# Kernel tuning notes

Measured on AMD Instinct MI355X. Metric: run time of the kernel, lower is better.

## Reference

```python
import jax, jax.numpy as jnp
import numpy as np

N_NODES, E_TOT, E_ACT = 20000, 250000, 200000
LAT, OH = 128, 128
M0, M1, M2 = 64, 32, 16            # irreps_out: 64x0e + 32x1o + 16x2e
D_IR = M0 + 3 * M1 + 5 * M2        # 240
G = M1 + M2                        # gate scalars (48)
T0 = M0 + G                        # tp m=0 scalar channels (112)
I0, I1, I2 = 3 * M0, 3 * M1, 3 * M2  # tp input muls (center|edge|neighbor)


def _split(x, m0, m1, m2):
    e = x.shape[0]
    return (x[:, :m0],
            x[:, m0:m0 + 3 * m1].reshape(e, m1, 3),
            x[:, m0 + 3 * m1:].reshape(e, m2, 5))


def _merge(s0, s1, s2):
    e = s0.shape[0]
    return jnp.concatenate([s0, s1.reshape(e, -1), s2.reshape(e, -1)], axis=-1)


def _mlp(x, ws, bs):
    for i, (w, b) in enumerate(zip(ws, bs)):
        x = x @ w + b
        if i < len(ws) - 1:
            x = jax.nn.silu(x)
    return x


def _forward(latents, node_features, edge_features, cutoff_coeffs, edge_one_hot,
             wigner_D1, wigner_D2,
             W0, W1r, W1i, W2r, W2i, Gw, Gb,
             P0, P0b, P1, P2, Ew, Eb, ln_g, ln_b,
             A1, A1b, A2, A2b, A3, A3b,
             B1, B1b, B2, B2b, B3, B3b,
             O0, O1, O2,
             edge_index, active_edges):
    ec = edge_index[0][active_edges]
    en = edge_index[1][active_edges]
    # gather node features per edge (equivariant_norm_type='none' -> identity norms)
    nc0, nc1, nc2 = _split(node_features[ec], M0, M1, M2)
    ef0, ef1, ef2 = _split(edge_features, M0, M1, M2)
    nn0, nn1, nn2 = _split(node_features[en], M0, M1, M2)
    x0 = jnp.concatenate([nc0, ef0, nn0], -1)   # [E,192]
    x1 = jnp.concatenate([nc1, ef1, nn1], 1)    # [E,96,3]
    x2 = jnp.concatenate([nc2, ef2, nn2], 1)    # [E,48,5]
    lat_a = latents[active_edges]
    # --- SO(2) linear: rotate into edge frame, per-m mixing, latent gains, rotate back ---
    r1 = jnp.einsum('eij,euj->eui', wigner_D1, x1)
    r2 = jnp.einsum('eij,euj->eui', wigner_D2, x2)
    in0 = jnp.concatenate([x0, r1[:, :, 1], r2[:, :, 2]], -1)   # m=0 [E,336]
    o_m0 = in0 @ W0.T                                           # [E,160]
    ip1 = jnp.concatenate([r1[:, :, 2], r2[:, :, 3]], -1)       # m=+1 [E,144]
    im1 = jnp.concatenate([r1[:, :, 0], r2[:, :, 1]], -1)       # m=-1
    op1 = ip1 @ W1r.T - im1 @ W1i.T                             # [E,48]
    on1 = ip1 @ W1i.T + im1 @ W1r.T
    op2 = r2[:, :, 4] @ W2r.T - r2[:, :, 0] @ W2i.T             # [E,16]
    on2 = r2[:, :, 4] @ W2i.T + r2[:, :, 0] @ W2r.T
    g = lat_a @ Gw + Gb                                         # per-edge gains [E,224]
    o_m0 = o_m0 * g[:, :160]
    g1 = g[:, 160:208]; g2 = g[:, 208:224]
    op1 = op1 * g1; on1 = on1 * g1; op2 = op2 * g2; on2 = on2 * g2
    y0 = o_m0[:, :T0]
    y1 = jnp.stack([on1[:, :M1], o_m0[:, T0:T0 + M1], op1[:, :M1]], -1)          # [E,32,3]
    y2 = jnp.stack([on2, on1[:, M1:], o_m0[:, T0 + M1:], op1[:, M1:], op2], -1)  # [E,16,5]
    y1 = jnp.einsum('eji,euj->eui', wigner_D1, y1)
    y2 = jnp.einsum('eji,euj->eui', wigner_D2, y2)
    # --- gate activation ---
    gates = jax.nn.sigmoid(y0[:, M0:])
    z0 = jax.nn.silu(y0[:, :M0])
    z1 = y1 * gates[:, :M1, None]
    z2 = y2 * gates[:, M1:, None]
    # --- lin_post: per-l channel mixing, fan-in normalized, bias on scalars ---
    z0 = z0 @ P0.T / np.sqrt(M0) + P0b
    z1 = jnp.einsum('uv,evm->eum', P1, z1) / np.sqrt(M1)
    z2 = jnp.einsum('uv,evm->eum', P2, z2) / np.sqrt(M2)
    scalars = z0                                               # taken before weighting
    # --- E3ElementLinear: per-edge per-channel weights from latents ---
    w = lat_a @ Ew + Eb                                        # [E,112]
    z0 = z0 * w[:, :M0]
    z1 = z1 * w[:, M0:M0 + M1, None]
    z2 = z2 * w[:, M0 + M1:, None]
    new_edge = _merge(z0, z1, z2)
    # --- latent update: LN -> mlp1(ln_lat||scalars) -> mlp2(h||one_hot) -> cutoff ---
    mu = lat_a.mean(-1, keepdims=True)
    var = ((lat_a - mu) ** 2).mean(-1, keepdims=True)
    ln_lat = (lat_a - mu) * jax.lax.rsqrt(var + 1e-5) * ln_g + ln_b
    h = _mlp(jnp.concatenate([ln_lat, scalars], -1), (A1, A2, A3), (A1b, A2b, A3b))
    h = _mlp(jnp.concatenate([h, edge_one_hot], -1), (B1, B2, B3), (B1b, B2b, B3b))
    new_lat = cutoff_coeffs[active_edges][:, None] * h
    # --- residual update (res_update_params buffer = 0) ---
    u = jax.nn.sigmoid(jnp.asarray(0.0, new_edge.dtype))
    c_old = jax.lax.rsqrt(u * u + 1.0)
    c_new = u * c_old
    edge_out = c_old * edge_features + c_new * new_edge        # identity residual path
    latents_out = latents.at[active_edges].set(c_new * new_lat + c_old * lat_a)
    # --- layer one-hot tensor product (uvu with 128x0e) ---
    f0, f1, f2 = _split(edge_out, M0, M1, M2)
    s = 1.0 / np.sqrt(OH)
    t0 = f0 * (edge_one_hot @ O0.T) * s
    t1 = f1 * (edge_one_hot @ O1.T)[:, :, None] * s
    t2 = f2 * (edge_one_hot @ O2.T)[:, :, None] * s
    edge_out = edge_out + _merge(t0, t1, t2)
    return edge_out, latents_out


def setup_inputs() -> dict:
    key = jax.random.key(0)
    ks = iter(jax.random.split(key, 64))
    nrm = lambda sh, s=0.05: jax.random.normal(next(ks), sh, jnp.float32) * s
    inp = dict(
        latents=nrm((E_TOT, LAT), 1.0),
        node_features=nrm((N_NODES, D_IR), 1.0),
        edge_features=nrm((E_ACT, D_IR), 1.0),
        cutoff_coeffs=jax.random.uniform(next(ks), (E_TOT,), jnp.float32),
        edge_one_hot=jax.random.uniform(next(ks), (E_ACT, OH), jnp.float32),
        wigner_D1=nrm((E_ACT, 3, 3), 0.5),
        wigner_D2=nrm((E_ACT, 5, 5), 0.3),
        W0=nrm((160, I0 + I1 + I2)), W1r=nrm((48, 144)), W1i=nrm((48, 144)),
        W2r=nrm((16, 48)), W2i=nrm((16, 48)),
        Gw=nrm((LAT, 224)), Gb=jnp.ones((224,), jnp.float32),
        P0=nrm((M0, M0)), P0b=nrm((M0,)), P1=nrm((M1, M1)), P2=nrm((M2, M2)),
        Ew=nrm((LAT, M0 + M1 + M2)), Eb=jnp.ones((M0 + M1 + M2,), jnp.float32),
        ln_g=jnp.ones((LAT,), jnp.float32), ln_b=jnp.zeros((LAT,), jnp.float32),
        A1=nrm((LAT + M0, LAT)), A1b=nrm((LAT,)),
        A2=nrm((LAT, LAT)), A2b=nrm((LAT,)),
        A3=nrm((LAT, LAT)), A3b=nrm((LAT,)),
        B1=nrm((LAT + OH, LAT)), B1b=nrm((LAT,)),
        B2=nrm((LAT, LAT)), B2b=nrm((LAT,)),
        B3=nrm((LAT, LAT)), B3b=nrm((LAT,)),
        O0=nrm((M0, OH)), O1=nrm((M1, OH)), O2=nrm((M2, OH)),
        edge_index=jax.random.randint(next(ks), (2, E_TOT), 0, N_NODES, jnp.int32),
        active_edges=jnp.sort(jax.random.permutation(next(ks), E_TOT)[:E_ACT]).astype(jnp.int32),
    )
    return inp


def reference(latents, node_features, edge_features, cutoff_coeffs, edge_one_hot,
              wigner_D1, wigner_D2,
              W0, W1r, W1i, W2r, W2i, Gw, Gb,
              P0, P0b, P1, P2, Ew, Eb, ln_g, ln_b,
              A1, A1b, A2, A2b, A3, A3b,
              B1, B1b, B2, B2b, B3, B3b,
              O0, O1, O2, edge_index, active_edges):
    return _forward(latents, node_features, edge_features, cutoff_coeffs, edge_one_hot,
                    wigner_D1, wigner_D2,
                    W0, W1r, W1i, W2r, W2i, Gw, Gb,
                    P0, P0b, P1, P2, Ew, Eb, ln_g, ln_b,
                    A1, A1b, A2, A2b, A3, A3b,
                    B1, B1b, B2, B2b, B3, B3b,
                    O0, O1, O2, edge_index, active_edges)
```

## Files before the change

### kernel.cpp

```cpp
#include <hip/hip_runtime.h>

typedef unsigned short us_t;
typedef short bf16x8 __attribute__((ext_vector_type(8)));
typedef float f32x4 __attribute__((ext_vector_type(4)));

#define E_ACT 200000
#define E_TOT 250000
#define DIR   240
#define C_OLD 0.8944271909999159f
#define C_NEW 0.4472135954999579f
#define S_OH  0.08838834764831845f

#define WO_W0   0
#define WO_W1P  56320
#define WO_W1M  70144
#define WO_W2P  83968
#define WO_W2M  85504
#define WO_GW   87040
#define WO_EW   115712
#define WO_A1   130048
#define WO_A2   154624
#define WO_A3   171008
#define WO_B1   187392
#define WO_B2   220160
#define WO_B3   236544
#define WO_O0   252928
#define WO_O1   261120
#define WO_O2   265216
#define WO_P0T  267264
#define WO_P1T  271360
#define WO_P2T  272384
#define W_TOTAL 272896

__device__ __forceinline__ float b2f(us_t u) { return __uint_as_float(((unsigned)u) << 16); }
__device__ __forceinline__ us_t f2b(float f) {
    unsigned x = __float_as_uint(f);
    return (us_t)((x + 0x7fffu + ((x >> 16) & 1u)) >> 16);
}
__device__ __forceinline__ float sigm(float x) { return 1.0f / (1.0f + __expf(-x)); }

#define MFMA(a,b,c) __builtin_amdgcn_mfma_f32_16x16x32_bf16((a),(b),(c),0,0,0)

__global__ __launch_bounds__(256) void prep_kernel(
    const float* __restrict__ W0, const float* __restrict__ W1r, const float* __restrict__ W1i,
    const float* __restrict__ W2r, const float* __restrict__ W2i,
    const float* __restrict__ Gw, const float* __restrict__ Ew,
    const float* __restrict__ A1, const float* __restrict__ A2, const float* __restrict__ A3,
    const float* __restrict__ B1, const float* __restrict__ B2, const float* __restrict__ B3,
    const float* __restrict__ O0, const float* __restrict__ O1, const float* __restrict__ O2,
    const float* __restrict__ P0w, const float* __restrict__ P1w, const float* __restrict__ P2w,
    us_t* __restrict__ wb)
{
    int idx = blockIdx.x * 256 + threadIdx.x;
    if (idx >= W_TOTAL) return;
    float v;
    if (idx < WO_W1P) {
        int r = idx, n = r / 352, k = r % 352;
        v = (k < 336) ? W0[n * 336 + k] : 0.f;
    } else if (idx < WO_W1M) {
        int r = idx - WO_W1P, n = r / 288, k = r % 288;
        v = (k < 144) ? W1r[n * 144 + k] : -W1i[n * 144 + (k - 144)];
    } else if (idx < WO_W2P) {
        int r = idx - WO_W1M, n = r / 288, k = r % 288;
        v = (k < 144) ? W1i[n * 144 + k] : W1r[n * 144 + (k - 144)];
    } else if (idx < WO_W2M) {
        int r = idx - WO_W2P, n = r / 96, k = r % 96;
        v = (k < 48) ? W2r[n * 48 + k] : -W2i[n * 48 + (k - 48)];
    } else if (idx < WO_GW) {
        int r = idx - WO_W2M, n = r / 96, k = r % 96;
        v = (k < 48) ? W2i[n * 48 + k] : W2r[n * 48 + (k - 48)];
    } else if (idx < WO_EW) {
        int r = idx - WO_GW, n = r / 128, k = r % 128;
        v = Gw[k * 224 + n];
    } else if (idx < WO_A1) {
        int r = idx - WO_EW, n = r / 128, k = r % 128;
        v = Ew[k * 112 + n];
    } else if (idx < WO_A2) {
        int r = idx - WO_A1, n = r / 192, k = r % 192;
        v = A1[k * 128 + n];
    } else if (idx < WO_A3) {
        int r = idx - WO_A2, n = r / 128, k = r % 128;
        v = A2[k * 128 + n];
    } else if (idx < WO_B1) {
        int r = idx - WO_A3, n = r / 128, k = r % 128;
        v = A3[k * 128 + n];
    } else if (idx < WO_B2) {
        int r = idx - WO_B1, n = r / 256, k = r % 256;
        v = B1[k * 128 + n];
    } else if (idx < WO_B3) {
        int r = idx - WO_B2, n = r / 128, k = r % 128;
        v = B2[k * 128 + n];
    } else if (idx < WO_O0) {
        int r = idx - WO_B3, n = r / 128, k = r % 128;
        v = B3[k * 128 + n];
    } else if (idx < WO_O1) {
        v = O0[idx - WO_O0];
    } else if (idx < WO_O2) {
        v = O1[idx - WO_O1];
    } else if (idx < WO_P0T) {
        v = O2[idx - WO_O2];
    } else if (idx < WO_P1T) {
        v = P0w[idx - WO_P0T];
    } else if (idx < WO_P2T) {
        v = P1w[idx - WO_P1T];
    } else {
        int r = idx - WO_P2T, n = r / 32, k = r % 32;
        v = (k < 16) ? P2w[n * 16 + k] : 0.f;
    }
    wb[idx] = f2b(v);
}

__global__ __launch_bounds__(256) void kcopy_kernel(
    const float* __restrict__ latents, const int* __restrict__ act,
    float* __restrict__ out_lat)
{
    int idx = blockIdx.x * 256 + threadIdx.x;
    if (idx >= E_TOT * 16) return;
    int row = idx >> 4, part = idx & 15;
    int lo = 0, hi = E_ACT;
    while (lo < hi) {
        int mid = (lo + hi) >> 1;
        if (act[mid] < row) lo = mid + 1; else hi = mid;
    }
    bool active = (lo < E_ACT) && (act[lo] == row);
    if (!active) {
        const float4* src = (const float4*)&latents[(size_t)row * 128 + part * 8];
        float4* dst = (float4*)&out_lat[(size_t)row * 128 + part * 8];
        dst[0] = src[0];
        dst[1] = src[1];
    }
}

__device__ __forceinline__ void lat_fetch_a(const float* __restrict__ latents,
                                            const int* __restrict__ aes_l,
                                            int lane, bf16x8 a[4])
{
    const int r = lane & 15, g = lane >> 4;
    const float* lp = latents + (size_t)aes_l[r] * 128 + g * 8;
    #pragma unroll
    for (int ks = 0; ks < 4; ++ks) {
        float4 v0 = *(const float4*)(lp + ks * 32);
        float4 v1 = *(const float4*)(lp + ks * 32 + 4);
        bf16x8 av;
        av[0] = (short)f2b(v0.x); av[1] = (short)f2b(v0.y);
        av[2] = (short)f2b(v0.z); av[3] = (short)f2b(v0.w);
        av[4] = (short)f2b(v1.x); av[5] = (short)f2b(v1.y);
        av[6] = (short)f2b(v1.z); av[7] = (short)f2b(v1.w);
        a[ks] = av;
    }
}

__device__ __forceinline__ void gemmW0g32(
    const us_t* __restrict__ in0s, const us_t* __restrict__ wbase,
    const bf16x8 lA[4], const bf16x8 lB[4], const float* __restrict__ Gb,
    int nt, us_t* __restrict__ om0g, int lane)
{
    const int r = lane & 15, g = lane >> 4;
    f32x4 wa = {0.f,0.f,0.f,0.f}, wb = wa, ga = wa, gb = wa;
    const us_t* apA = in0s + r * 360 + g * 8;
    const us_t* apB = in0s + (16 + r) * 360 + g * 8;
    const us_t* wp  = wbase + WO_W0 + (size_t)(nt * 16 + r) * 352 + g * 8;
    #pragma unroll
    for (int ks = 0; ks < 11; ++ks) {
        bf16x8 b = *(const bf16x8*)(wp + ks * 32);
        wa = MFMA(*(const bf16x8*)(apA + ks * 32), b, wa);
        wb = MFMA(*(const bf16x8*)(apB + ks * 32), b, wb);
    }
    const us_t* gp = wbase + WO_GW + (size_t)(nt * 16 + r) * 128 + g * 8;
    #pragma unroll
    for (int ks = 0; ks < 4; ++ks) {
        bf16x8 b = *(const bf16x8*)(gp + ks * 32);
        ga = MFMA(lA[ks], b, ga);
        gb = MFMA(lB[ks], b, gb);
    }
    float bi = Gb[nt * 16 + r];
    #pragma unroll
    for (int i = 0; i < 4; ++i) {
        int eA = g * 4 + i, eB = 16 + g * 4 + i;
        om0g[eA * 162 + nt * 16 + r] = f2b(wa[i] * (ga[i] + bi));
        om0g[eB * 162 + nt * 16 + r] = f2b(wb[i] * (gb[i] + bi));
    }
}

__device__ __forceinline__ void gemmW1g32(
    const us_t* __restrict__ cact1, const us_t* __restrict__ wbase,
    const bf16x8 lA[4], const bf16x8 lB[4], const float* __restrict__ Gb,
    int j, us_t* __restrict__ cp1g, us_t* __restrict__ cn1g, int lane)
{
    const int r = lane & 15, g = lane >> 4;
    f32x4 pa = {0.f,0.f,0.f,0.f}, pb = pa, ma = pa, mb = pa, ga = pa, gb = pa;
    const us_t* apA = cact1 + r * 296 + g * 8;
    const us_t* apB = cact1 + (16 + r) * 296 + g * 8;
    const us_t* wpP = wbase + WO_W1P + (size_t)(j * 16 + r) * 288 + g * 8;
    const us_t* wpM = wbase + WO_W1M + (size_t)(j * 16 + r) * 288 + g * 8;
    #pragma unroll
    for (int ks = 0; ks < 9; ++ks) {
        bf16x8 aA = *(const bf16x8*)(apA + ks * 32);
        bf16x8 aB = *(const bf16x8*)(apB + ks * 32);
        bf16x8 bP = *(const bf16x8*)(wpP + ks * 32);
        bf16x8 bM = *(const bf16x8*)(wpM + ks * 32);
        pa = MFMA(aA, bP, pa); pb = MFMA(aB, bP, pb);
        ma = MFMA(aA, bM, ma); mb = MFMA(aB, bM, mb);
    }
    const us_t* gp = wbase + WO_GW + (size_t)(160 + j * 16 + r) * 128 + g * 8;
    #pragma unroll
    for (int ks = 0; ks < 4; ++ks) {
        bf16x8 b = *(const bf16x8*)(gp + ks * 32);
        ga = MFMA(lA[ks], b, ga);
        gb = MFMA(lB[ks], b, gb);
    }
    float bi = Gb[160 + j * 16 + r];
    #pragma unroll
    for (int i = 0; i < 4; ++i) {
        int eA = g * 4 + i, eB = 16 + g * 4 + i;
        float gA = ga[i] + bi, gB = gb[i] + bi;
        cp1g[eA * 50 + j * 16 + r] = f2b(pa[i] * gA);
        cn1g[eA * 50 + j * 16 + r] = f2b(ma[i] * gA);
        cp1g[eB * 50 + j * 16 + r] = f2b(pb[i] * gB);
        cn1g[eB * 50 + j * 16 + r] = f2b(mb[i] * gB);
    }
}

__device__ __forceinline__ void gemmW2g32(
    const us_t* __restrict__ cact2, const us_t* __restrict__ wbase,
    const bf16x8 lA[4], const bf16x8 lB[4], const float* __restrict__ Gb,
    us_t* __restrict__ cp2g, us_t* __restrict__ cn2g, int lane)
{
    const int r = lane & 15, g = lane >> 4;
    f32x4 pa = {0.f,0.f,0.f,0.f}, pb = pa, ma = pa, mb = pa, ga = pa, gb = pa;
    const us_t* apA = cact2 + r * 104 + g * 8;
    const us_t* apB = cact2 + (16 + r) * 104 + g * 8;
    const us_t* wpP = wbase + WO_W2P + (size_t)r * 96 + g * 8;
    const us_t* wpM = wbase + WO_W2M + (size_t)r * 96 + g * 8;
    #pragma unroll
    for (int ks = 0; ks < 3; ++ks) {
        bf16x8 aA = *(const bf16x8*)(apA + ks * 32);
        bf16x8 aB = *(const bf16x8*)(apB + ks * 32);
        bf16x8 bP = *(const bf16x8*)(wpP + ks * 32);
        bf16x8 bM = *(const bf16x8*)(wpM + ks * 32);
        pa = MFMA(aA, bP, pa); pb = MFMA(aB, bP, pb);
        ma = MFMA(aA, bM, ma); mb = MFMA(aB, bM, mb);
    }
    const us_t* gp = wbase + WO_GW + (size_t)(208 + r) * 128 + g * 8;
    #pragma unroll
    for (int ks = 0; ks < 4; ++ks) {
        bf16x8 b = *(const bf16x8*)(gp + ks * 32);
        ga = MFMA(lA[ks], b, ga);
        gb = MFMA(lB[ks], b, gb);
    }
    float bi = Gb[208 + r];
    #pragma unroll
    for (int i = 0; i < 4; ++i) {
        int eA = g * 4 + i, eB = 16 + g * 4 + i;
        float gA = ga[i] + bi, gB = gb[i] + bi;
        cp2g[eA * 18 + r] = f2b(pa[i] * gA);
        cn2g[eA * 18 + r] = f2b(ma[i] * gA);
        cp2g[eB * 18 + r] = f2b(pb[i] * gB);
        cn2g[eB * 18 + r] = f2b(mb[i] * gB);
    }
}

__device__ __forceinline__ void lat_gemmE32(
    const bf16x8 lA[4], const bf16x8 lB[4],
    const us_t* __restrict__ wgt, const float* __restrict__ bias,
    int nt, us_t* __restrict__ wl, int lane)
{
    const int r = lane & 15, g = lane >> 4;
    f32x4 aA = {0.f,0.f,0.f,0.f}, aB = aA;
    const us_t* wp = wgt + (size_t)(nt * 16 + r) * 128 + g * 8;
    #pragma unroll
    for (int ks = 0; ks < 4; ++ks) {
        bf16x8 b = *(const bf16x8*)(wp + ks * 32);
        aA = MFMA(lA[ks], b, aA);
        aB = MFMA(lB[ks], b, aB);
    }
    float bi = bias[nt * 16 + r];
    #pragma unroll
    for (int i = 0; i < 4; ++i) {
        int eA = g * 4 + i, eB = 16 + g * 4 + i;
        wl[eA * 120 + nt * 16 + r] = f2b(aA[i] + bi);
        wl[eB * 120 + nt * 16 + r] = f2b(aB[i] + bi);
    }
}

template<int KS>
__device__ __forceinline__ void pgemm32(const us_t* __restrict__ actbase, int as,
                                        const us_t* __restrict__ wgt, int kp, int lane,
                                        f32x4& accA, f32x4& accB)
{
    const int r = lane & 15, g = lane >> 4;
    const us_t* apA = actbase + r * as + g * 8;
    const us_t* apB = actbase + (16 + r) * as + g * 8;
    const us_t* wp = wgt + (size_t)r * kp + g * 8;
    #pragma unroll
    for (int ks = 0; ks < KS; ++ks) {
        bf16x8 b = *(const bf16x8*)(wp + ks * 32);
        accA = MFMA(*(const bf16x8*)(apA + ks * 32), b, accA);
        accB = MFMA(*(const bf16x8*)(apB + ks * 32), b, accB);
    }
}

template<int KS, bool SILU>
__device__ __forceinline__ void mlayer(
    const us_t* __restrict__ actA, const us_t* __restrict__ actB, int split, int as,
    const us_t* __restrict__ wgt, int kp, const float* __restrict__ bias,
    us_t* __restrict__ out, int os, int lane, int w)
{
    const int r = lane & 15, g = lane >> 4;
    const int n0 = 2 * w * 16, n1 = n0 + 16;
    f32x4 a00 = {0.f,0.f,0.f,0.f}, a01 = a00, a10 = a00, a11 = a00;
    const us_t* wp0 = wgt + (size_t)(n0 + r) * kp + g * 8;
    const us_t* wp1 = wgt + (size_t)(n1 + r) * kp + g * 8;
    #pragma unroll
    for (int ks = 0; ks < KS; ++ks) {
        const us_t* ab = (ks < split) ? (actA + ks * 32) : (actB + (ks - split) * 32);
        bf16x8 f0 = *(const bf16x8*)(ab + r * as + g * 8);
        bf16x8 f1 = *(const bf16x8*)(ab + (16 + r) * as + g * 8);
        bf16x8 b0 = *(const bf16x8*)(wp0 + ks * 32);
        bf16x8 b1 = *(const bf16x8*)(wp1 + ks * 32);
        a00 = MFMA(f0, b0, a00); a01 = MFMA(f0, b1, a01);
        a10 = MFMA(f1, b0, a10); a11 = MFMA(f1, b1, a11);
    }
    float bi0 = bias[n0 + r], bi1 = bias[n1 + r];
    #pragma unroll
    for (int i = 0; i < 4; ++i) {
        int eA = g * 4 + i, eB = 16 + g * 4 + i;
        float v;
        v = a00[i] + bi0; if (SILU) v *= sigm(v); out[eA * os + n0 + r] = f2b(v);
        v = a01[i] + bi1; if (SILU) v *= sigm(v); out[eA * os + n1 + r] = f2b(v);
        v = a10[i] + bi0; if (SILU) v *= sigm(v); out[eB * os + n0 + r] = f2b(v);
        v = a11[i] + bi1; if (SILU) v *= sigm(v); out[eB * os + n1 + r] = f2b(v);
    }
}

__global__ __launch_bounds__(256, 2) void fused_kernel(
    const float* __restrict__ latents,
    const float* __restrict__ node_features,
    const float* __restrict__ edge_features,
    const float* __restrict__ cutoff,
    const float* __restrict__ one_hot,
    const float* __restrict__ wD1,
    const float* __restrict__ wD2,
    const float* __restrict__ Gb,  const float* __restrict__ Eb,
    const float* __restrict__ P0b,
    const float* __restrict__ ln_g, const float* __restrict__ ln_b,
    const float* __restrict__ A1b, const float* __restrict__ A2b, const float* __restrict__ A3b,
    const float* __restrict__ B1b, const float* __restrict__ B2b, const float* __restrict__ B3b,
    const int* __restrict__ edge_index, const int* __restrict__ active_edges,
    const us_t* __restrict__ wbase,
    us_t* __restrict__ ne_ws,
    float* __restrict__ out_edge, float* __restrict__ out_lat)
{
    __shared__ __align__(16) char smem[80640];
    us_t* in0s  = (us_t*)(smem);
    us_t* cact1 = (us_t*)(smem + 23040);
    us_t* cact2 = (us_t*)(smem + 41984);
    us_t* z0l   = (us_t*)(smem);
    us_t* z1l   = (us_t*)(smem + 4608);
    us_t* z2l   = (us_t*)(smem + 11264);
    us_t* x_lds = (us_t*)(smem);
    us_t* h_a   = (us_t*)(smem + 12800);
    us_t* h_b   = (us_t*)(smem + 21504);
    us_t* ohl   = (us_t*)(smem + 30208);
    us_t* ohw_l = (us_t*)(smem + 38912);
    float* D1l  = (float*)(smem + 48640);
    float* D2l  = (float*)(smem + 50176);
    int*   aes  = (int*)(smem + 53760);
    us_t* om0g  = (us_t*)(smem + 53888);
    us_t* cp1g  = (us_t*)(smem + 64256);
    us_t* cn1g  = (us_t*)(smem + 67456);
    us_t* cp2g  = (us_t*)(smem + 70656);
    us_t* cn2g  = (us_t*)(smem + 71808);
    us_t* wl    = (us_t*)(smem + 72960);
    us_t* scal_l= (us_t*)(smem + 64256);
    float* cut_l= (float*)(smem + 53888);

    const int t  = threadIdx.x;
    const int e0 = blockIdx.x * 32;
    const int lane = t & 63, w = t >> 6;

    #pragma unroll
    for (int ep = 0; ep < 2; ++ep) {
        const int e = (t >> 4) + 16 * ep, l = t & 15;
        const int eg = e0 + e;
        const int ae = active_edges[eg];
        const int ec = edge_index[ae];
        const int en = edge_index[E_TOT + ae];
        if (l == 0) aes[e] = ae;

        float v1  = (l < 9) ? wD1[(size_t)eg * 9 + l] : 0.f;
        float v2a = wD2[(size_t)eg * 25 + l];
        float v2b = (l < 9) ? wD2[(size_t)eg * 25 + 16 + l] : 0.f;
        if (l < 9) D1l[e * 12 + l] = v1;
        D2l[e * 28 + l] = v2a;
        if (l < 9) D2l[e * 28 + 16 + l] = v2b;

        float d1[9], d2[25];
        #pragma unroll
        for (int i = 0; i < 9; ++i)  d1[i] = __shfl(v1, i, 16);
        #pragma unroll
        for (int i = 0; i < 16; ++i) d2[i] = __shfl(v2a, i, 16);
        #pragma unroll
        for (int i = 0; i < 9; ++i)  d2[16 + i] = __shfl(v2b, i, 16);

        const float* pc = node_features + (size_t)ec * DIR;
        const float* pe = edge_features + (size_t)eg * DIR;
        const float* pn = node_features + (size_t)en * DIR;
        us_t* in0 = in0s + e * 360;
        us_t* c1  = cact1 + e * 296;
        us_t* c2  = cact2 + e * 104;

        #pragma unroll
        for (int j = 0; j < 4; ++j) {
            int i = l + 16 * j;
            in0[i]       = f2b(pc[i]);
            in0[64 + i]  = f2b(pe[i]);
            in0[128 + i] = f2b(pn[i]);
        }
        in0[336 + l] = 0;

        #pragma unroll
        for (int jj = 0; jj < 6; ++jj) {
            int u = l + 16 * jj;
            int uu = u & 31;
            const float* sp = (u < 32 ? pc : (u < 64 ? pe : pn)) + 64 + uu * 3;
            float x0 = sp[0], x1 = sp[1], x2 = sp[2];
            float r0 = d1[0] * x0 + d1[1] * x1 + d1[2] * x2;
            float r1 = d1[3] * x0 + d1[4] * x1 + d1[5] * x2;
            float r2 = d1[6] * x0 + d1[7] * x1 + d1[8] * x2;
            c1[144 + u]  = f2b(r0);
            in0[192 + u] = f2b(r1);
            c1[u]        = f2b(r2);
        }
        #pragma unroll
        for (int jj = 0; jj < 3; ++jj) {
            int u = l + 16 * jj;
            int uu = u & 15;
            const float* sp = (u < 16 ? pc : (u < 32 ? pe : pn)) + 160 + uu * 5;
            float x0 = sp[0], x1 = sp[1], x2 = sp[2], x3 = sp[3], x4 = sp[4];
            float r[5];
            #pragma unroll
            for (int i = 0; i < 5; ++i)
                r[i] = d2[i * 5 + 0] * x0 + d2[i * 5 + 1] * x1 + d2[i * 5 + 2] * x2
                     + d2[i * 5 + 3] * x3 + d2[i * 5 + 4] * x4;
            c2[48 + u]   = f2b(r[0]);
            c1[240 + u]  = f2b(r[1]);
            in0[288 + u] = f2b(r[2]);
            c1[96 + u]   = f2b(r[3]);
            c2[u]        = f2b(r[4]);
        }
    }
    __syncthreads();

    {
        bf16x8 lA[4], lB[4];
        lat_fetch_a(latents, aes, lane, lA);
        lat_fetch_a(latents, aes + 16, lane, lB);
        if (w == 0) {
            gemmW0g32(in0s, wbase, lA, lB, Gb, 0, om0g, lane);
            gemmW0g32(in0s, wbase, lA, lB, Gb, 1, om0g, lane);
            gemmW0g32(in0s, wbase, lA, lB, Gb, 2, om0g, lane);
            gemmW1g32(cact1, wbase, lA, lB, Gb, 0, cp1g, cn1g, lane);
        } else if (w == 1) {
            gemmW0g32(in0s, wbase, lA, lB, Gb, 3, om0g, lane);
            gemmW0g32(in0s, wbase, lA, lB, Gb, 4, om0g, lane);
            gemmW0g32(in0s, wbase, lA, lB, Gb, 5, om0g, lane);
            gemmW1g32(cact1, wbase, lA, lB, Gb, 1, cp1g, cn1g, lane);
        } else if (w == 2) {
            gemmW0g32(in0s, wbase, lA, lB, Gb, 6, om0g, lane);
            gemmW0g32(in0s, wbase, lA, lB, Gb, 7, om0g, lane);
            gemmW0g32(in0s, wbase, lA, lB, Gb, 8, om0g, lane);
            gemmW1g32(cact1, wbase, lA, lB, Gb, 2, cp1g, cn1g, lane);
        } else {
            gemmW0g32(in0s, wbase, lA, lB, Gb, 9, om0g, lane);
            gemmW2g32(cact2, wbase, lA, lB, Gb, cp2g, cn2g, lane);
            #pragma unroll
            for (int nt = 0; nt < 7; ++nt)
                lat_gemmE32(lA, lB, wbase + WO_EW, Eb, nt, wl, lane);
        }
    }
    __syncthreads();

    #pragma unroll
    for (int ep = 0; ep < 2; ++ep) {
        const int e = (t >> 4) + 16 * ep, l = t & 15;
        const float* D1e = D1l + e * 12;
        const float* D2e = D2l + e * 28;
        #pragma unroll
        for (int uu = 0; uu < 2; ++uu) {
            int u = l + uu * 16;
            float j0 = b2f(cn1g[e * 50 + u]);
            float j1 = b2f(om0g[e * 162 + 112 + u]);
            float j2 = b2f(cp1g[e * 50 + u]);
            float gate = sigm(b2f(om0g[e * 162 + 64 + u]));
            #pragma unroll
            for (int i = 0; i < 3; ++i) {
                float yr = D1e[0 * 3 + i] * j0 + D1e[1 * 3 + i] * j1 + D1e[2 * 3 + i] * j2;
                z1l[e * 104 + i * 32 + u] = f2b(yr * gate);
            }
        }
        {
            int u = l;
            float j0 = b2f(cn2g[e * 18 + u]);
            float j1 = b2f(cn1g[e * 50 + 32 + u]);
            float j2 = b2f(om0g[e * 162 + 144 + u]);
            float j3 = b2f(cp1g[e * 50 + 32 + u]);
            float j4 = b2f(cp2g[e * 18 + u]);
            float gate = sigm(b2f(om0g[e * 162 + 96 + u]));
            #pragma unroll
            for (int i = 0; i < 5; ++i) {
                float yr = D2e[0 * 5 + i] * j0 + D2e[1 * 5 + i] * j1 + D2e[2 * 5 + i] * j2
                         + D2e[3 * 5 + i] * j3 + D2e[4 * 5 + i] * j4;
                z2l[e * 168 + i * 32 + u] = f2b(yr * gate);
                z2l[e * 168 + i * 32 + 16 + u] = 0;
            }
        }
        #pragma unroll
        for (int ii = 0; ii < 4; ++ii) {
            int c = l + 16 * ii;
            float v = b2f(om0g[e * 162 + c]);
            z0l[e * 72 + c] = f2b(v * sigm(v));
        }
    }
    __syncthreads();

    {
        const int r = lane & 15, g = lane >> 4;
        const float sc1 = 0.17677669529663687f;
        if (w < 2) {
            #pragma unroll
            for (int jj = 0; jj < 2; ++jj) {
                int nt = 2 * w + jj;
                f32x4 aA = {0.f,0.f,0.f,0.f}, aB = aA;
                pgemm32<2>(z0l, 72, wbase + WO_P0T + nt * 16 * 64, 64, lane, aA, aB);
                int n = nt * 16 + r;
                float bi = P0b[n];
                #pragma unroll
                for (int i = 0; i < 4; ++i) {
                    int eA = g * 4 + i, eB = 16 + g * 4 + i;
                    float zA = aA[i] * 0.125f + bi;
                    float zB = aB[i] * 0.125f + bi;
                    scal_l[eA * 64 + n] = f2b(zA);
                    scal_l[eB * 64 + n] = f2b(zB);
                    ne_ws[(size_t)(e0 + eA) * 240 + n] = f2b(zA * b2f(wl[eA * 120 + n]));
                    ne_ws[(size_t)(e0 + eB) * 240 + n] = f2b(zB * b2f(wl[eB * 120 + n]));
                }
            }
        } else if (w == 2) {
            #pragma unroll
            for (int m = 0; m < 3; ++m) {
                #pragma unroll
                for (int nt = 0; nt < 2; ++nt) {
                    f32x4 aA = {0.f,0.f,0.f,0.f}, aB = aA;
                    pgemm32<1>(z1l + m * 32, 104, wbase + WO_P1T + nt * 16 * 32, 32,
                               lane, aA, aB);
                    int u = nt * 16 + r;
                    #pragma unroll
                    for (int i = 0; i < 4; ++i) {
                        int eA = g * 4 + i, eB = 16 + g * 4 + i;
                        ne_ws[(size_t)(e0 + eA) * 240 + 64 + u * 3 + m] =
                            f2b(aA[i] * sc1 * b2f(wl[eA * 120 + 64 + u]));
                        ne_ws[(size_t)(e0 + eB) * 240 + 64 + u * 3 + m] =
                            f2b(aB[i] * sc1 * b2f(wl[eB * 120 + 64 + u]));
                    }
                }
            }
        } else if (w == 3) {
            #pragma unroll
            for (int m = 0; m < 5; ++m) {
                f32x4 aA = {0.f,0.f,0.f,0.f}, aB = aA;
                pgemm32<1>(z2l + m * 32, 168, wbase + WO_P2T, 32, lane, aA, aB);
                int u = r;
                #pragma unroll
                for (int i = 0; i < 4; ++i) {
                    int eA = g * 4 + i, eB = 16 + g * 4 + i;
                    ne_ws[(size_t)(e0 + eA) * 240 + 160 + u * 5 + m] =
                        f2b(aA[i] * 0.25f * b2f(wl[eA * 120 + 96 + u]));
                    ne_ws[(size_t)(e0 + eB) * 240 + 160 + u * 5 + m] =
                        f2b(aB[i] * 0.25f * b2f(wl[eB * 120 + 96 + u]));
                }
            }
        }
    }
    __syncthreads();

    {
        int ee = t >> 3, l8 = t & 7;
        int ae = aes[ee];
        if (l8 == 0) cut_l[ee] = cutoff[ae];
        const float* lp = latents + (size_t)ae * 128 + l8 * 16;
        float xs[16];
        #pragma unroll
        for (int q = 0; q < 4; ++q) {
            float4 v = *(const float4*)(lp + q * 4);
            xs[q * 4 + 0] = v.x; xs[q * 4 + 1] = v.y;
            xs[q * 4 + 2] = v.z; xs[q * 4 + 3] = v.w;
        }
        float s1 = 0.f, s2 = 0.f;
        #pragma unroll
        for (int i = 0; i < 16; ++i) { s1 += xs[i]; s2 += xs[i] * xs[i]; }
        #pragma unroll
        for (int off = 1; off < 8; off <<= 1) {
            s1 += __shfl_xor(s1, off, 8);
            s2 += __shfl_xor(s2, off, 8);
        }
        float mu  = s1 * (1.f / 128.f);
        float var = s2 * (1.f / 128.f) - mu * mu;
        float rstd = rsqrtf(var + 1e-5f);
        #pragma unroll
        for (int i = 0; i < 16; ++i) {
            int li = l8 * 16 + i;
            x_lds[ee * 200 + li] = f2b((xs[i] - mu) * rstd * ln_g[li] + ln_b[li]);
        }
        #pragma unroll
        for (int q = 0; q < 2; ++q) {
            int j = l8 * 2 + q;
            *(ushort4*)&x_lds[ee * 200 + 128 + j * 4] =
                *(const ushort4*)&scal_l[ee * 64 + j * 4];
        }
    }
    for (int idx = t; idx < 32 * 32; idx += 256) {
        int ee = idx >> 5, j = idx & 31;
        float4 ov = *(const float4*)&one_hot[(size_t)(e0 + ee) * 128 + j * 4];
        ushort4 s; s.x = f2b(ov.x); s.y = f2b(ov.y); s.z = f2b(ov.z); s.w = f2b(ov.w);
        *(ushort4*)&ohl[ee * 136 + j * 4] = s;
    }
    __syncthreads();

    mlayer<6, true>(x_lds, x_lds, 6, 200, wbase + WO_A1, 192, A1b, h_a, 136, lane, w);
    __syncthreads();
    mlayer<4, true>(h_a, h_a, 4, 136, wbase + WO_A2, 128, A2b, h_b, 136, lane, w);
    __syncthreads();
    mlayer<4, false>(h_b, h_b, 4, 136, wbase + WO_A3, 128, A3b, h_a, 136, lane, w);
    __syncthreads();
    mlayer<8, true>(h_a, ohl, 4, 136, wbase + WO_B1, 256, B1b, h_b, 136, lane, w);
    __syncthreads();
    mlayer<4, true>(h_b, h_b, 4, 136, wbase + WO_B2, 128, B2b, h_a, 136, lane, w);
    __syncthreads();

    {
        const int r = lane & 15, g = lane >> 4;
        const int n0 = 2 * w * 16, n1 = n0 + 16;
        f32x4 a00 = {0.f,0.f,0.f,0.f}, a01 = a00, a10 = a00, a11 = a00;
        const us_t* wp0 = wbase + WO_B3 + (size_t)(n0 + r) * 128 + g * 8;
        const us_t* wp1 = wbase + WO_B3 + (size_t)(n1 + r) * 128 + g * 8;
        #pragma unroll
        for (int ks = 0; ks < 4; ++ks) {
            bf16x8 f0 = *(const bf16x8*)(h_a + ks * 32 + r * 136 + g * 8);
            bf16x8 f1 = *(const bf16x8*)(h_a + ks * 32 + (16 + r) * 136 + g * 8);
            bf16x8 b0 = *(const bf16x8*)(wp0 + ks * 32);
            bf16x8 b1 = *(const bf16x8*)(wp1 + ks * 32);
            a00 = MFMA(f0, b0, a00); a01 = MFMA(f0, b1, a01);
            a10 = MFMA(f1, b0, a10); a11 = MFMA(f1, b1, a11);
        }
        float bi0 = B3b[n0 + r], bi1 = B3b[n1 + r];
        #pragma unroll
        for (int i = 0; i < 4; ++i) {
            int eA = g * 4 + i, eB = 16 + g * 4 + i;
            int aeA = aes[eA], aeB = aes[eB];
            float cA = C_NEW * cut_l[eA], cB = C_NEW * cut_l[eB];
            float* oA = out_lat + (size_t)aeA * 128;
            float* oB = out_lat + (size_t)aeB * 128;
            const float* lA = latents + (size_t)aeA * 128;
            const float* lB = latents + (size_t)aeB * 128;
            oA[n0 + r] = cA * (a00[i] + bi0) + C_OLD * lA[n0 + r];
            oA[n1 + r] = cA * (a01[i] + bi1) + C_OLD * lA[n1 + r];
            oB[n0 + r] = cB * (a10[i] + bi0) + C_OLD * lB[n0 + r];
            oB[n1 + r] = cB * (a11[i] + bi1) + C_OLD * lB[n1 + r];
        }
    }
    {
        const int r = lane & 15, g = lane >> 4;
        const int cnt = (w == 3) ? 1 : 2;
        #pragma unroll
        for (int ii = 0; ii < 2; ++ii) {
            if (ii >= cnt) break;
            int nt = (ii == 0) ? w : w + 4;
            const us_t* wb2 = (nt < 4) ? (wbase + WO_O0 + (size_t)nt * 16 * 128)
                            : (nt < 6) ? (wbase + WO_O1 + (size_t)(nt - 4) * 16 * 128)
                                       : (wbase + WO_O2);
            f32x4 c0 = {0.f,0.f,0.f,0.f}, c1 = c0;
            const us_t* wp = wb2 + (size_t)r * 128 + g * 8;
            #pragma unroll
            for (int ks = 0; ks < 4; ++ks) {
                bf16x8 f0 = *(const bf16x8*)(ohl + ks * 32 + r * 136 + g * 8);
                bf16x8 f1 = *(const bf16x8*)(ohl + ks * 32 + (16 + r) * 136 + g * 8);
                bf16x8 b = *(const bf16x8*)(wp + ks * 32);
                c0 = MFMA(f0, b, c0); c1 = MFMA(f1, b, c1);
            }
            int n = nt * 16 + r;
            #pragma unroll
            for (int i = 0; i < 4; ++i) {
                int eA = g * 4 + i, eB = 16 + g * 4 + i;
                ohw_l[eA * 112 + n] = f2b(c0[i]);
                ohw_l[eB * 112 + n] = f2b(c1[i]);
            }
        }
    }
    __syncthreads();

    for (int idx = t; idx < 32 * 60; idx += 256) {
        int e = idx / 60;
        int c0 = (idx - e * 60) * 4;
        size_t eg = (size_t)(e0 + e);
        float4 ef = *(const float4*)&edge_features[eg * 240 + c0];
        ushort4 nv = *(const ushort4*)&ne_ws[eg * 240 + c0];
        float nef[4] = {b2f(nv.x), b2f(nv.y), b2f(nv.z), b2f(nv.w)};
        float eff[4] = {ef.x, ef.y, ef.z, ef.w};
        float4 ov;
        float* op = &ov.x;
        #pragma unroll
        for (int j = 0; j < 4; ++j) {
            int c = c0 + j;
            int o;
            if (c < 64)       o = c;
            else if (c < 160) o = 64 + (c - 64) / 3;
            else              o = 96 + (c - 160) / 5;
            float ohv = b2f(ohw_l[e * 112 + o]);
            op[j] = (C_OLD * eff[j] + C_NEW * nef[j]) * (1.f + S_OH * ohv);
        }
        *(float4*)&out_edge[eg * 240 + c0] = ov;
    }
}

extern "C" void kernel_launch(void* const* d_in, const int* in_sizes, int n_in,
                              void* d_out, int out_size, void* d_ws, size_t ws_size,
                              hipStream_t stream)
{
    const float* latents  = (const float*)d_in[0];
    const float* node_f   = (const float*)d_in[1];
    const float* edge_f   = (const float*)d_in[2];
    const float* cutoff   = (const float*)d_in[3];
    const float* one_hot  = (const float*)d_in[4];
    const float* wD1      = (const float*)d_in[5];
    const float* wD2      = (const float*)d_in[6];
    const float* W0       = (const float*)d_in[7];
    const float* W1r      = (const float*)d_in[8];
    const float* W1i      = (const float*)d_in[9];
    const float* W2r      = (const float*)d_in[10];
    const float* W2i      = (const float*)d_in[11];
    const float* Gw       = (const float*)d_in[12];
    const float* Gb       = (const float*)d_in[13];
    const float* P0w      = (const float*)d_in[14];
    const float* P0b      = (const float*)d_in[15];
    const float* P1w      = (const float*)d_in[16];
    const float* P2w      = (const float*)d_in[17];
    const float* Ew       = (const float*)d_in[18];
    const float* Eb       = (const float*)d_in[19];
    const float* ln_g     = (const float*)d_in[20];
    const float* ln_b     = (const float*)d_in[21];
    const float* A1       = (const float*)d_in[22];
    const float* A1b      = (const float*)d_in[23];
    const float* A2       = (const float*)d_in[24];
    const float* A2b      = (const float*)d_in[25];
    const float* A3       = (const float*)d_in[26];
    const float* A3b      = (const float*)d_in[27];
    const float* B1       = (const float*)d_in[28];
    const float* B1b      = (const float*)d_in[29];
    const float* B2       = (const float*)d_in[30];
    const float* B2b      = (const float*)d_in[31];
    const float* B3       = (const float*)d_in[32];
    const float* B3b      = (const float*)d_in[33];
    const float* O0       = (const float*)d_in[34];
    const float* O1       = (const float*)d_in[35];
    const float* O2       = (const float*)d_in[36];
    const int* edge_index = (const int*)d_in[37];
    const int* act_e      = (const int*)d_in[38];

    float* out_edge = (float*)d_out;
    float* out_lat  = out_edge + (size_t)E_ACT * DIR;

    us_t* ne_ws   = (us_t*)d_ws;
    us_t* wbase   = ne_ws + (size_t)E_ACT * DIR;

    prep_kernel<<<dim3((W_TOTAL + 255) / 256), dim3(256), 0, stream>>>(
        W0, W1r, W1i, W2r, W2i, Gw, Ew, A1, A2, A3, B1, B2, B3,
        O0, O1, O2, P0w, P1w, P2w, wbase);

    kcopy_kernel<<<dim3((E_TOT * 16 + 255) / 256), dim3(256), 0, stream>>>(
        latents, act_e, out_lat);

    fused_kernel<<<dim3(E_ACT / 32), dim3(256), 0, stream>>>(
        latents, node_f, edge_f, cutoff, one_hot, wD1, wD2,
        Gb, Eb, P0b, ln_g, ln_b,
        A1b, A2b, A3b, B1b, B2b, B3b,
        edge_index, act_e, wbase, ne_ws, out_edge, out_lat);
}
```

Measured before the change: 699.3 us.

## Double fused kernel block to 512 threads and redistribute per-wave GEMM work

The fused kernel now runs 8 waves per 32-edge block instead of 4. Each phase (gather/rotate, SO(2) GEMMs, projection GEMMs, layernorm, MLP layers, output heads) is re-partitioned so each wave handles fewer N-tiles or edges, and launch bounds move to (512,4). The goal is more parallelism within each block and lower per-wave register pressure, so latency is better hidden. The cost is that each block still uses about 80 KB of LDS, which limits how many blocks fit per CU, and some phases leave waves poorly balanced.

```diff
diff --git a/kernel.cpp b/kernel.cpp
--- a/kernel.cpp
+++ b/kernel.cpp
@@ -301,39 +301,35 @@
 }
 
 template<int KS, bool SILU>
-__device__ __forceinline__ void mlayer(
+__device__ __forceinline__ void mlayer8(
     const us_t* __restrict__ actA, const us_t* __restrict__ actB, int split, int as,
     const us_t* __restrict__ wgt, int kp, const float* __restrict__ bias,
     us_t* __restrict__ out, int os, int lane, int w)
 {
     const int r = lane & 15, g = lane >> 4;
-    const int n0 = 2 * w * 16, n1 = n0 + 16;
-    f32x4 a00 = {0.f,0.f,0.f,0.f}, a01 = a00, a10 = a00, a11 = a00;
-    const us_t* wp0 = wgt + (size_t)(n0 + r) * kp + g * 8;
-    const us_t* wp1 = wgt + (size_t)(n1 + r) * kp + g * 8;
+    const int n0 = w * 16;
+    f32x4 a0 = {0.f,0.f,0.f,0.f}, a1 = a0;
+    const us_t* wp = wgt + (size_t)(n0 + r) * kp + g * 8;
     #pragma unroll
     for (int ks = 0; ks < KS; ++ks) {
         const us_t* ab = (ks < split) ? (actA + ks * 32) : (actB + (ks - split) * 32);
         bf16x8 f0 = *(const bf16x8*)(ab + r * as + g * 8);
         bf16x8 f1 = *(const bf16x8*)(ab + (16 + r) * as + g * 8);
-        bf16x8 b0 = *(const bf16x8*)(wp0 + ks * 32);
-        bf16x8 b1 = *(const bf16x8*)(wp1 + ks * 32);
-        a00 = MFMA(f0, b0, a00); a01 = MFMA(f0, b1, a01);
-        a10 = MFMA(f1, b0, a10); a11 = MFMA(f1, b1, a11);
-    }
-    float bi0 = bias[n0 + r], bi1 = bias[n1 + r];
+        bf16x8 b = *(const bf16x8*)(wp + ks * 32);
+        a0 = MFMA(f0, b, a0);
+        a1 = MFMA(f1, b, a1);
+    }
+    float bi = bias[n0 + r];
     #pragma unroll
     for (int i = 0; i < 4; ++i) {
         int eA = g * 4 + i, eB = 16 + g * 4 + i;
         float v;
-        v = a00[i] + bi0; if (SILU) v *= sigm(v); out[eA * os + n0 + r] = f2b(v);
-        v = a01[i] + bi1; if (SILU) v *= sigm(v); out[eA * os + n1 + r] = f2b(v);
-        v = a10[i] + bi0; if (SILU) v *= sigm(v); out[eB * os + n0 + r] = f2b(v);
-        v = a11[i] + bi1; if (SILU) v *= sigm(v); out[eB * os + n1 + r] = f2b(v);
-    }
-}
-
-__global__ __launch_bounds__(256, 2) void fused_kernel(
+        v = a0[i] + bi; if (SILU) v *= sigm(v); out[eA * os + n0 + r] = f2b(v);
+        v = a1[i] + bi; if (SILU) v *= sigm(v); out[eB * os + n0 + r] = f2b(v);
+    }
+}
+
+__global__ __launch_bounds__(512, 4) void fused_kernel(
     const float* __restrict__ latents,
     const float* __restrict__ node_features,
     const float* __restrict__ edge_features,
@@ -379,9 +375,8 @@
     const int e0 = blockIdx.x * 32;
     const int lane = t & 63, w = t >> 6;
 
-    #pragma unroll
-    for (int ep = 0; ep < 2; ++ep) {
-        const int e = (t >> 4) + 16 * ep, l = t & 15;
+    {
+        const int e = t >> 4, l = t & 15;
         const int eg = e0 + e;
         const int ae = active_edges[eg];
         const int ec = edge_index[ae];
@@ -456,24 +451,16 @@
         bf16x8 lA[4], lB[4];
         lat_fetch_a(latents, aes, lane, lA);
         lat_fetch_a(latents, aes + 16, lane, lB);
-        if (w == 0) {
-            gemmW0g32(in0s, wbase, lA, lB, Gb, 0, om0g, lane);
-            gemmW0g32(in0s, wbase, lA, lB, Gb, 1, om0g, lane);
-            gemmW0g32(in0s, wbase, lA, lB, Gb, 2, om0g, lane);
+        if (w < 5) {
+            gemmW0g32(in0s, wbase, lA, lB, Gb, 2 * w, om0g, lane);
+            gemmW0g32(in0s, wbase, lA, lB, Gb, 2 * w + 1, om0g, lane);
+        } else if (w == 5) {
             gemmW1g32(cact1, wbase, lA, lB, Gb, 0, cp1g, cn1g, lane);
-        } else if (w == 1) {
-            gemmW0g32(in0s, wbase, lA, lB, Gb, 3, om0g, lane);
-            gemmW0g32(in0s, wbase, lA, lB, Gb, 4, om0g, lane);
-            gemmW0g32(in0s, wbase, lA, lB, Gb, 5, om0g, lane);
             gemmW1g32(cact1, wbase, lA, lB, Gb, 1, cp1g, cn1g, lane);
-        } else if (w == 2) {
-            gemmW0g32(in0s, wbase, lA, lB, Gb, 6, om0g, lane);
-            gemmW0g32(in0s, wbase, lA, lB, Gb, 7, om0g, lane);
-            gemmW0g32(in0s, wbase, lA, lB, Gb, 8, om0g, lane);
+        } else if (w == 6) {
             gemmW1g32(cact1, wbase, lA, lB, Gb, 2, cp1g, cn1g, lane);
+            gemmW2g32(cact2, wbase, lA, lB, Gb, cp2g, cn2g, lane);
         } else {
-            gemmW0g32(in0s, wbase, lA, lB, Gb, 9, om0g, lane);
-            gemmW2g32(cact2, wbase, lA, lB, Gb, cp2g, cn2g, lane);
             #pragma unroll
             for (int nt = 0; nt < 7; ++nt)
                 lat_gemmE32(lA, lB, wbase + WO_EW, Eb, nt, wl, lane);
@@ -481,9 +468,8 @@
     }
     __syncthreads();
 
-    #pragma unroll
-    for (int ep = 0; ep < 2; ++ep) {
-        const int e = (t >> 4) + 16 * ep, l = t & 15;
+    {
+        const int e = t >> 4, l = t & 15;
         const float* D1e = D1l + e * 12;
         const float* D2e = D2l + e * 28;
         #pragma unroll
@@ -527,47 +513,44 @@
     {
         const int r = lane & 15, g = lane >> 4;
         const float sc1 = 0.17677669529663687f;
-        if (w < 2) {
+        if (w < 4) {
+            f32x4 aA = {0.f,0.f,0.f,0.f}, aB = aA;
+            pgemm32<2>(z0l, 72, wbase + WO_P0T + w * 16 * 64, 64, lane, aA, aB);
+            int n = w * 16 + r;
+            float bi = P0b[n];
             #pragma unroll
-            for (int jj = 0; jj < 2; ++jj) {
-                int nt = 2 * w + jj;
+            for (int i = 0; i < 4; ++i) {
+                int eA = g * 4 + i, eB = 16 + g * 4 + i;
+                float zA = aA[i] * 0.125f + bi;
+                float zB = aB[i] * 0.125f + bi;
+                scal_l[eA * 64 + n] = f2b(zA);
+                scal_l[eB * 64 + n] = f2b(zB);
+                ne_ws[(size_t)(e0 + eA) * 240 + n] = f2b(zA * b2f(wl[eA * 120 + n]));
+                ne_ws[(size_t)(e0 + eB) * 240 + n] = f2b(zB * b2f(wl[eB * 120 + n]));
+            }
+        } else if (w == 4 || w == 5) {
+            #pragma unroll
+            for (int q = 0; q < 3; ++q) {
+                int idx = (w - 4) * 3 + q;
+                int m = idx >> 1, nt = idx & 1;
                 f32x4 aA = {0.f,0.f,0.f,0.f}, aB = aA;
-                pgemm32<2>(z0l, 72, wbase + WO_P0T + nt * 16 * 64, 64, lane, aA, aB);
-                int n = nt * 16 + r;
-                float bi = P0b[n];
+                pgemm32<1>(z1l + m * 32, 104, wbase + WO_P1T + nt * 16 * 32, 32,
+                           lane, aA, aB);
+                int u = nt * 16 + r;
                 #pragma unroll
                 for (int i = 0; i < 4; ++i) {
                     int eA = g * 4 + i, eB = 16 + g * 4 + i;
-                    float zA = aA[i] * 0.125f + bi;
-                    float zB = aB[i] * 0.125f + bi;
-                    scal_l[eA * 64 + n] = f2b(zA);
-                    scal_l[eB * 64 + n] = f2b(zB);
-                    ne_ws[(size_t)(e0 + eA) * 240 + n] = f2b(zA * b2f(wl[eA * 120 + n]));
-                    ne_ws[(size_t)(e0 + eB) * 240 + n] = f2b(zB * b2f(wl[eB * 120 + n]));
+                    ne_ws[(size_t)(e0 + eA) * 240 + 64 + u * 3 + m] =
+                        f2b(aA[i] * sc1 * b2f(wl[eA * 120 + 64 + u]));
+                    ne_ws[(size_t)(e0 + eB) * 240 + 64 + u * 3 + m] =
+                        f2b(aB[i] * sc1 * b2f(wl[eB * 120 + 64 + u]));
                 }
             }
-        } else if (w == 2) {
-            #pragma unroll
-            for (int m = 0; m < 3; ++m) {
-                #pragma unroll
-                for (int nt = 0; nt < 2; ++nt) {
-                    f32x4 aA = {0.f,0.f,0.f,0.f}, aB = aA;
-                    pgemm32<1>(z1l + m * 32, 104, wbase + WO_P1T + nt * 16 * 32, 32,
-                               lane, aA, aB);
-                    int u = nt * 16 + r;
-                    #pragma unroll
-                    for (int i = 0; i < 4; ++i) {
-                        int eA = g * 4 + i, eB = 16 + g * 4 + i;
-                        ne_ws[(size_t)(e0 + eA) * 240 + 64 + u * 3 + m] =
-                            f2b(aA[i] * sc1 * b2f(wl[eA * 120 + 64 + u]));
-                        ne_ws[(size_t)(e0 + eB) * 240 + 64 + u * 3 + m] =
-                            f2b(aB[i] * sc1 * b2f(wl[eB * 120 + 64 + u]));
-                    }
-                }
-            }
-        } else if (w == 3) {
-            #pragma unroll
-            for (int m = 0; m < 5; ++m) {
+        } else {
+            const int mstart = (w == 6) ? 0 : 3;
+            const int mcnt   = (w == 6) ? 3 : 2;
+            for (int q = 0; q < mcnt; ++q) {
+                int m = mstart + q;
                 f32x4 aA = {0.f,0.f,0.f,0.f}, aB = aA;
                 pgemm32<1>(z2l + m * 32, 168, wbase + WO_P2T, 32, lane, aA, aB);
                 int u = r;
@@ -585,41 +568,33 @@
     __syncthreads();
 
     {
-        int ee = t >> 3, l8 = t & 7;
+        int ee = t >> 4, l16 = t & 15;
         int ae = aes[ee];
-        if (l8 == 0) cut_l[ee] = cutoff[ae];
-        const float* lp = latents + (size_t)ae * 128 + l8 * 16;
-        float xs[16];
-        #pragma unroll
-        for (int q = 0; q < 4; ++q) {
-            float4 v = *(const float4*)(lp + q * 4);
-            xs[q * 4 + 0] = v.x; xs[q * 4 + 1] = v.y;
-            xs[q * 4 + 2] = v.z; xs[q * 4 + 3] = v.w;
-        }
+        if (l16 == 0) cut_l[ee] = cutoff[ae];
+        const float* lp = latents + (size_t)ae * 128 + l16 * 8;
+        float4 va = *(const float4*)lp;
+        float4 vb = *(const float4*)(lp + 4);
+        float xs[8] = {va.x, va.y, va.z, va.w, vb.x, vb.y, vb.z, vb.w};
         float s1 = 0.f, s2 = 0.f;
         #pragma unroll
-        for (int i = 0; i < 16; ++i) { s1 += xs[i]; s2 += xs[i] * xs[i]; }
-        #pragma unroll
-        for (int off = 1; off < 8; off <<= 1) {
-            s1 += __shfl_xor(s1, off, 8);
-            s2 += __shfl_xor(s2, off, 8);
+        for (int i = 0; i < 8; ++i) { s1 += xs[i]; s2 += xs[i] * xs[i]; }
+        #pragma unroll
+        for (int off = 1; off < 16; off <<= 1) {
+            s1 += __shfl_xor(s1, off, 16);
+            s2 += __shfl_xor(s2, off, 16);
         }
         float mu  = s1 * (1.f / 128.f);
         float var = s2 * (1.f / 128.f) - mu * mu;
         float rstd = rsqrtf(var + 1e-5f);
         #pragma unroll
-        for (int i = 0; i < 16; ++i) {
-            int li = l8 * 16 + i;
+        for (int i = 0; i < 8; ++i) {
+            int li = l16 * 8 + i;
             x_lds[ee * 200 + li] = f2b((xs[i] - mu) * rstd * ln_g[li] + ln_b[li]);
         }
-        #pragma unroll
-        for (int q = 0; q < 2; ++q) {
-            int j = l8 * 2 + q;
-            *(ushort4*)&x_lds[ee * 200 + 128 + j * 4] =
-                *(const ushort4*)&scal_l[ee * 64 + j * 4];
-        }
-    }
-    for (int idx = t; idx < 32 * 32; idx += 256) {
+        *(ushort4*)&x_lds[ee * 200 + 128 + l16 * 4] =
+            *(const ushort4*)&scal_l[ee * 64 + l16 * 4];
+    }
+    for (int idx = t; idx < 32 * 32; idx += 512) {
         int ee = idx >> 5, j = idx & 31;
         float4 ov = *(const float4*)&one_hot[(size_t)(e0 + ee) * 128 + j * 4];
         ushort4 s; s.x = f2b(ov.x); s.y = f2b(ov.y); s.z = f2b(ov.z); s.w = f2b(ov.w);
@@ -627,79 +602,68 @@
     }
     __syncthreads();
 
-    mlayer<6, true>(x_lds, x_lds, 6, 200, wbase + WO_A1, 192, A1b, h_a, 136, lane, w);
-    __syncthreads();
-    mlayer<4, true>(h_a, h_a, 4, 136, wbase + WO_A2, 128, A2b, h_b, 136, lane, w);
-    __syncthreads();
-    mlayer<4, false>(h_b, h_b, 4, 136, wbase + WO_A3, 128, A3b, h_a, 136, lane, w);
-    __syncthreads();
-    mlayer<8, true>(h_a, ohl, 4, 136, wbase + WO_B1, 256, B1b, h_b, 136, lane, w);
-    __syncthreads();
-    mlayer<4, true>(h_b, h_b, 4, 136, wbase + WO_B2, 128, B2b, h_a, 136, lane, w);
+    mlayer8<6, true>(x_lds, x_lds, 6, 200, wbase + WO_A1, 192, A1b, h_a, 136, lane, w);
+    __syncthreads();
+    mlayer8<4, true>(h_a, h_a, 4, 136, wbase + WO_A2, 128, A2b, h_b, 136, lane, w);
+    __syncthreads();
+    mlayer8<4, false>(h_b, h_b, 4, 136, wbase + WO_A3, 128, A3b, h_a, 136, lane, w);
+    __syncthreads();
+    mlayer8<8, true>(h_a, ohl, 4, 136, wbase + WO_B1, 256, B1b, h_b, 136, lane, w);
+    __syncthreads();
+    mlayer8<4, true>(h_b, h_b, 4, 136, wbase + WO_B2, 128, B2b, h_a, 136, lane, w);
     __syncthreads();
 
     {
         const int r = lane & 15, g = lane >> 4;
-        const int n0 = 2 * w * 16, n1 = n0 + 16;
-        f32x4 a00 = {0.f,0.f,0.f,0.f}, a01 = a00, a10 = a00, a11 = a00;
-        const us_t* wp0 = wbase + WO_B3 + (size_t)(n0 + r) * 128 + g * 8;
-        const us_t* wp1 = wbase + WO_B3 + (size_t)(n1 + r) * 128 + g * 8;
+        const int n0 = w * 16;
+        f32x4 a0 = {0.f,0.f,0.f,0.f}, a1 = a0;
+        const us_t* wp = wbase + WO_B3 + (size_t)(n0 + r) * 128 + g * 8;
         #pragma unroll
         for (int ks = 0; ks < 4; ++ks) {
             bf16x8 f0 = *(const bf16x8*)(h_a + ks * 32 + r * 136 + g * 8);
             bf16x8 f1 = *(const bf16x8*)(h_a + ks * 32 + (16 + r) * 136 + g * 8);
-            bf16x8 b0 = *(const bf16x8*)(wp0 + ks * 32);
-            bf16x8 b1 = *(const bf16x8*)(wp1 + ks * 32);
-            a00 = MFMA(f0, b0, a00); a01 = MFMA(f0, b1, a01);
-            a10 = MFMA(f1, b0, a10); a11 = MFMA(f1, b1, a11);
-        }
-        float bi0 = B3b[n0 + r], bi1 = B3b[n1 + r];
+            bf16x8 b = *(const bf16x8*)(wp + ks * 32);
+            a0 = MFMA(f0, b, a0);
+            a1 = MFMA(f1, b, a1);
+        }
+        float bi = B3b[n0 + r];
         #pragma unroll
         for (int i = 0; i < 4; ++i) {
             int eA = g * 4 + i, eB = 16 + g * 4 + i;
             int aeA = aes[eA], aeB = aes[eB];
             float cA = C_NEW * cut_l[eA], cB = C_NEW * cut_l[eB];
-            float* oA = out_lat + (size_t)aeA * 128;
-            float* oB = out_lat + (size_t)aeB * 128;
-            const float* lA = latents + (size_t)aeA * 128;
-            const float* lB = latents + (size_t)aeB * 128;
-            oA[n0 + r] = cA * (a00[i] + bi0) + C_OLD * lA[n0 + r];
-            oA[n1 + r] = cA * (a01[i] + bi1) + C_OLD * lA[n1 + r];
-            oB[n0 + r] = cB * (a10[i] + bi0) + C_OLD * lB[n0 + r];
-            oB[n1 + r] = cB * (a11[i] + bi1) + C_OLD * lB[n1 + r];
-        }
-    }
-    {
+            out_lat[(size_t)aeA * 128 + n0 + r] =
+                cA * (a0[i] + bi) + C_OLD * latents[(size_t)aeA * 128 + n0 + r];
+            out_lat[(size_t)aeB * 128 + n0 + r] =
+                cB * (a1[i] + bi) + C_OLD * latents[(size_t)aeB * 128 + n0 + r];
+        }
+    }
+    if (w < 7) {
         const int r = lane & 15, g = lane >> 4;
-        const int cnt = (w == 3) ? 1 : 2;
-        #pragma unroll
-        for (int ii = 0; ii < 2; ++ii) {
-            if (ii >= cnt) break;
-            int nt = (ii == 0) ? w : w + 4;
-            const us_t* wb2 = (nt < 4) ? (wbase + WO_O0 + (size_t)nt * 16 * 128)
-                            : (nt < 6) ? (wbase + WO_O1 + (size_t)(nt - 4) * 16 * 128)
-                                       : (wbase + WO_O2);
-            f32x4 c0 = {0.f,0.f,0.f,0.f}, c1 = c0;
-            const us_t* wp = wb2 + (size_t)r * 128 + g * 8;
-            #pragma unroll
-            for (int ks = 0; ks < 4; ++ks) {
-                bf16x8 f0 = *(const bf16x8*)(ohl + ks * 32 + r * 136 + g * 8);
-                bf16x8 f1 = *(const bf16x8*)(ohl + ks * 32 + (16 + r) * 136 + g * 8);
-                bf16x8 b = *(const bf16x8*)(wp + ks * 32);
-                c0 = MFMA(f0, b, c0); c1 = MFMA(f1, b, c1);
-            }
-            int n = nt * 16 + r;
-            #pragma unroll
-            for (int i = 0; i < 4; ++i) {
-                int eA = g * 4 + i, eB = 16 + g * 4 + i;
-                ohw_l[eA * 112 + n] = f2b(c0[i]);
-                ohw_l[eB * 112 + n] = f2b(c1[i]);
-            }
-        }
-    }
-    __syncthreads();
-
-    for (int idx = t; idx < 32 * 60; idx += 256) {
+        const int nt = w;
+        const us_t* wb2 = (nt < 4) ? (wbase + WO_O0 + (size_t)nt * 16 * 128)
+                        : (nt < 6) ? (wbase + WO_O1 + (size_t)(nt - 4) * 16 * 128)
+                                   : (wbase + WO_O2);
+        f32x4 c0 = {0.f,0.f,0.f,0.f}, c1 = c0;
+        const us_t* wp = wb2 + (size_t)r * 128 + g * 8;
+        #pragma unroll
+        for (int ks = 0; ks < 4; ++ks) {
+            bf16x8 f0 = *(const bf16x8*)(ohl + ks * 32 + r * 136 + g * 8);
+            bf16x8 f1 = *(const bf16x8*)(ohl + ks * 32 + (16 + r) * 136 + g * 8);
+            bf16x8 b = *(const bf16x8*)(wp + ks * 32);
+            c0 = MFMA(f0, b, c0); c1 = MFMA(f1, b, c1);
+        }
+        int n = nt * 16 + r;
+        #pragma unroll
+        for (int i = 0; i < 4; ++i) {
+            int eA = g * 4 + i, eB = 16 + g * 4 + i;
+            ohw_l[eA * 112 + n] = f2b(c0[i]);
+            ohw_l[eB * 112 + n] = f2b(c1[i]);
+        }
+    }
+    __syncthreads();
+
+    for (int idx = t; idx < 32 * 60; idx += 512) {
         int e = idx / 60;
         int c0 = (idx - e * 60) * 4;
         size_t eg = (size_t)(e0 + e);
@@ -780,7 +744,7 @@
     kcopy_kernel<<<dim3((E_TOT * 16 + 255) / 256), dim3(256), 0, stream>>>(
         latents, act_e, out_lat);
 
-    fused_kernel<<<dim3(E_ACT / 32), dim3(256), 0, stream>>>(
+    fused_kernel<<<dim3(E_ACT / 32), dim3(512), 0, stream>>>(
         latents, node_f, edge_f, cutoff, one_hot, wD1, wD2,
         Gb, Eb, P0b, ln_g, ln_b,
         A1b, A2b, A3b, B1b, B2b, B3b,
```

Measured after the change: 763.3 us. 9.2% more time.
